# Optimization experiments

Measured on AMD Instinct MI355X. Metric: run time of the kernel, lower is better.

Reference implementation:

```python
import jax, jax.numpy as jnp
import numpy as np

T, B, I, H, L = 1024, 64, 512, 512, 2


def _gru_layer(x_seq, h0, w_ih, w_hh, b_ih, b_hh):
    # x_seq: [T, B, in], h0: [B, H]
    # Precompute input-side gates for all timesteps in one big GEMM.
    gx = jnp.einsum('tbi,gi->tbg', x_seq, w_ih) + b_ih  # [T, B, 3H]

    def step(h, gx_t):
        gh = h @ w_hh.T + b_hh                 # [B, 3H]
        i_r, i_z, i_n = jnp.split(gx_t, 3, axis=-1)
        h_r, h_z, h_n = jnp.split(gh, 3, axis=-1)
        r = jax.nn.sigmoid(i_r + h_r)
        z = jax.nn.sigmoid(i_z + h_z)
        n = jnp.tanh(i_n + r * h_n)
        hy = n + z * (h - n)                   # newgate + inputgate*(hx - newgate)
        return hy, hy

    hT, out = jax.lax.scan(step, h0, gx)
    return out, hT  # out: [T, B, H]


def setup_inputs() -> dict:
    key = jax.random.key(0)
    ks = jax.random.split(key, 10)
    stdv = 1.0 / np.sqrt(H)
    u = lambda k, shp: jax.random.uniform(k, shp, jnp.float32, -stdv, stdv)
    return {
        'x': jax.random.normal(ks[0], (T, B, I), jnp.float32),
        'hx': jax.random.normal(ks[1], (L, B, H), jnp.float32),
        'w_ih_0': u(ks[2], (3 * H, I)),
        'w_hh_0': u(ks[3], (3 * H, H)),
        'b_ih_0': u(ks[4], (3 * H,)),
        'b_hh_0': u(ks[5], (3 * H,)),
        'w_ih_1': u(ks[6], (3 * H, H)),
        'w_hh_1': u(ks[7], (3 * H, H)),
        'b_ih_1': u(ks[8], (3 * H,)),
        'b_hh_1': u(ks[9], (3 * H,)),
    }


def reference(x, hx, w_ih_0, w_hh_0, b_ih_0, b_hh_0, w_ih_1, w_hh_1, b_ih_1, b_hh_1):
    out0, h0T = _gru_layer(x, hx[0], w_ih_0, w_hh_0, b_ih_0, b_hh_0)
    out1, h1T = _gru_layer(out0, hx[1], w_ih_1, w_hh_1, b_ih_1, b_hh_1)
    output = out1                         # [T, B, H] (batch_first=False)
    output_hs = jnp.stack([h0T, h1T], 0)  # [L, B, H]
    return output, output_hs
```

## Files before the change

kernel.cpp:

```cpp
#include <hip/hip_runtime.h>
#include <cstdint>
#include <cstddef>

#define T_N 1024
#define B_N 64
#define I_N 512
#define H_N 512
#define G3  (3*H_N)
#define NBLK 256

typedef _Float16 f16;
typedef _Float16 f16x2 __attribute__((ext_vector_type(2)));

__device__ __forceinline__ f16x2 mkh2(float a, float b) {
  f16x2 v; v.x = (_Float16)a; v.y = (_Float16)b; return v;
}
__device__ __forceinline__ f16x2 bch2(unsigned int u) {
  return __builtin_bit_cast(f16x2, u);
}
__device__ __forceinline__ float fdot2_(f16x2 a, f16x2 b, float c) {
#if __has_builtin(__builtin_amdgcn_fdot2)
  return __builtin_amdgcn_fdot2(a, b, c, false);
#else
  return fmaf((float)a.x, (float)b.x, fmaf((float)a.y, (float)b.y, c));
#endif
}
__device__ __forceinline__ float sigm_(float x) { return 1.f / (1.f + __expf(-x)); }

__global__ __launch_bounds__(256) void gemm_nt(
    const float* __restrict__ A,
    const float* __restrict__ W,
    const float* __restrict__ bias,
    float* __restrict__ C,
    int M, int N, int K)
{
  __shared__ float As[32][68];
  __shared__ float Ws[32][68];
  const int tid = threadIdx.x;
  const int n0 = blockIdx.x * 64;
  const int m0 = blockIdx.y * 64;
  const int ty = tid >> 4;
  const int tx = tid & 15;

  float acc[4][4];
#pragma unroll
  for (int i = 0; i < 4; ++i)
#pragma unroll
    for (int j = 0; j < 4; ++j) acc[i][j] = 0.f;

  for (int k0 = 0; k0 < K; k0 += 32) {
#pragma unroll
    for (int i = 0; i < 2; ++i) {
      int idx = tid + i * 256;
      int r   = idx >> 3;
      int c4  = idx & 7;
      float4 va = *(const float4*)(A + (size_t)(m0 + r) * K + k0 + c4 * 4);
      As[c4*4+0][r] = va.x; As[c4*4+1][r] = va.y;
      As[c4*4+2][r] = va.z; As[c4*4+3][r] = va.w;
      float4 vw = *(const float4*)(W + (size_t)(n0 + r) * K + k0 + c4 * 4);
      Ws[c4*4+0][r] = vw.x; Ws[c4*4+1][r] = vw.y;
      Ws[c4*4+2][r] = vw.z; Ws[c4*4+3][r] = vw.w;
    }
    __syncthreads();
#pragma unroll
    for (int k = 0; k < 32; ++k) {
      float4 a = *(const float4*)&As[k][ty * 4];
      float4 w = *(const float4*)&Ws[k][tx * 4];
      acc[0][0] += a.x*w.x; acc[0][1] += a.x*w.y; acc[0][2] += a.x*w.z; acc[0][3] += a.x*w.w;
      acc[1][0] += a.y*w.x; acc[1][1] += a.y*w.y; acc[1][2] += a.y*w.z; acc[1][3] += a.y*w.w;
      acc[2][0] += a.z*w.x; acc[2][1] += a.z*w.y; acc[2][2] += a.z*w.z; acc[2][3] += a.z*w.w;
      acc[3][0] += a.w*w.x; acc[3][1] += a.w*w.y; acc[3][2] += a.w*w.z; acc[3][3] += a.w*w.w;
    }
    __syncthreads();
  }

  float4 bv = *(const float4*)(bias + n0 + tx * 4);
#pragma unroll
  for (int i = 0; i < 4; ++i) {
    int row = m0 + ty * 4 + i;
    float4 o;
    o.x = acc[i][0] + bv.x; o.y = acc[i][1] + bv.y;
    o.z = acc[i][2] + bv.z; o.w = acc[i][3] + bv.w;
    *(float4*)(C + (size_t)row * N + n0 + tx * 4) = o;
  }
}

__global__ __launch_bounds__(256) void pack_h_init(
    const float* __restrict__ hx, f16* h0x1, f16* h1x1)
{
  int i = blockIdx.x * 256 + threadIdx.x;
  h0x1[i] = (f16)hx[i];
  h1x1[i] = (f16)hx[B_N * H_N + i];
}

__global__ __launch_bounds__(256, 1) void gru_fused(
    const float* __restrict__ gx,
    const float* __restrict__ hx,
    const float* wih1, const float* whh0, const float* whh1,
    const float* bih1, const float* bhh0, const float* bhh1,
    float* __restrict__ out,
    float* __restrict__ hT,
    f16* h0x, f16* h1x,
    int* flags0, int* flags1)
{
  __shared__ f16 sh0[8 * 512];
  __shared__ f16 sh1[8 * 512];
  __shared__ float red[512 * 36];
  __shared__ __align__(8) unsigned short pk[128];

  const int tid = threadIdx.x;
  const int bid = blockIdx.x;
  const int g   = bid & 7;
  const int j   = bid >> 3;
  const int up  = tid >> 5;
  const int s   = tid & 31;

  f16x2 wA[3][2][8];
  f16x2 wX[3][2][8];
  f16x2 wH[3][2][8];
#pragma unroll
  for (int q = 0; q < 3; ++q)
#pragma unroll
    for (int e = 0; e < 2; ++e) {
      const size_t row = (size_t)(q * H_N + 16 * j + 2 * up + e);
      const float* pA = whh0 + row * H_N;
      const float* pX = wih1 + row * H_N;
      const float* pH = whh1 + row * H_N;
#pragma unroll
      for (int c = 0; c < 4; ++c) {
        const int k0 = 8 * s + 2 * c;
        const int k1 = 256 + 8 * s + 2 * c;
        wA[q][e][c]     = mkh2(pA[k0], pA[k0 + 1]);
        wA[q][e][4 + c] = mkh2(pA[k1], pA[k1 + 1]);
        wX[q][e][c]     = mkh2(pX[k0], pX[k0 + 1]);
        wX[q][e][4 + c] = mkh2(pX[k1], pX[k1 + 1]);
        wH[q][e][c]     = mkh2(pH[k0], pH[k0 + 1]);
        wH[q][e][4 + c] = mkh2(pH[k1], pH[k1 + 1]);
      }
    }

  const int gu = tid & 15;
  const int gb8 = tid >> 4;
  float bR0=0,bZ0=0,bN0=0, xR1=0,xZ1=0,xN1=0, hR1=0,hZ1=0,hN1=0, hv0=0, hv1=0;
  if (tid < 128) {
    const int unit = 16 * j + gu;
    const int gbi  = 8 * g + gb8;
    bR0 = bhh0[unit]; bZ0 = bhh0[H_N + unit]; bN0 = bhh0[2 * H_N + unit];
    xR1 = bih1[unit]; xZ1 = bih1[H_N + unit]; xN1 = bih1[2 * H_N + unit];
    hR1 = bhh1[unit]; hZ1 = bhh1[H_N + unit]; hN1 = bhh1[2 * H_N + unit];
    hv0 = hx[(size_t)gbi * H_N + unit];
    hv1 = hx[(size_t)(B_N + gbi) * H_N + unit];
  }

  for (int t = 0; t <= T_N; ++t) {
    float ir0 = 0, iz0 = 0, in0 = 0;
    if (t < T_N && tid < 128) {
      const float* p = gx + ((size_t)t * B_N + 8 * g + gb8) * G3 + 16 * j + gu;
      ir0 = p[0]; iz0 = p[H_N]; in0 = p[2 * H_N];
    }

    if (t > 0) {
      if (tid < 64) {
        int* fp = (tid < 32) ? (flags0 + (8 * tid + g) * 16)
                             : (flags1 + (8 * (tid - 32) + g) * 16);
        const int need = (tid < 32) ? t : (t - 1);
        int spin = 0;
        for (;;) {
          int f = __hip_atomic_load(fp, __ATOMIC_RELAXED, __HIP_MEMORY_SCOPE_AGENT);
          if (__all(f >= need)) break;
          __builtin_amdgcn_s_sleep(1);
          if ((++spin & 1023) == 1023)
            __builtin_amdgcn_fence(__ATOMIC_ACQUIRE, "agent");
        }
      }
      __builtin_amdgcn_sched_barrier(0);
      __syncthreads();
    }

    {
      unsigned long long* s0 = (unsigned long long*)(h0x + (size_t)((t - 1) & 1) * (B_N * H_N) + (size_t)(8 * g) * H_N);
      unsigned long long* s1 = (unsigned long long*)(h1x + (size_t)((t - 2) & 1) * (B_N * H_N) + (size_t)(8 * g) * H_N);
      unsigned long long* d0 = (unsigned long long*)sh0;
      unsigned long long* d1 = (unsigned long long*)sh1;
#pragma unroll
      for (int e = 0; e < 4; ++e) {
        d0[e * 256 + tid] = __hip_atomic_load(s0 + e * 256 + tid, __ATOMIC_RELAXED, __HIP_MEMORY_SCOPE_AGENT);
        d1[e * 256 + tid] = __hip_atomic_load(s1 + e * 256 + tid, __ATOMIC_RELAXED, __HIP_MEMORY_SCOPE_AGENT);
      }
    }
    __syncthreads();

    if (t < T_N) {
      float acc[3][2][8];
#pragma unroll
      for (int q = 0; q < 3; ++q)
#pragma unroll
        for (int e = 0; e < 2; ++e)
#pragma unroll
          for (int bb = 0; bb < 8; ++bb) acc[q][e][bb] = 0.f;

#pragma unroll
      for (int bb = 0; bb < 8; ++bb) {
        uint4 u0 = *(const uint4*)&sh0[bb * 512 + 8 * s];
        uint4 u1 = *(const uint4*)&sh0[bb * 512 + 256 + 8 * s];
        f16x2 h[8] = {bch2(u0.x), bch2(u0.y), bch2(u0.z), bch2(u0.w),
                      bch2(u1.x), bch2(u1.y), bch2(u1.z), bch2(u1.w)};
#pragma unroll
        for (int e = 0; e < 2; ++e) {
          float ar = acc[0][e][bb], az = acc[1][e][bb], an = acc[2][e][bb];
#pragma unroll
          for (int c = 0; c < 8; ++c) {
            ar = fdot2_(wA[0][e][c], h[c], ar);
            az = fdot2_(wA[1][e][c], h[c], az);
            an = fdot2_(wA[2][e][c], h[c], an);
          }
          acc[0][e][bb] = ar; acc[1][e][bb] = az; acc[2][e][bb] = an;
        }
      }
#pragma unroll
      for (int q = 0; q < 3; ++q)
#pragma unroll
        for (int e = 0; e < 2; ++e)
#pragma unroll
          for (int bb = 0; bb < 8; ++bb)
            red[((2 * up + e) + 16 * (q * 8 + bb)) * 36 + s] = acc[q][e][bb];
      __syncthreads();

      if (tid < 128) {
        float sg[3];
#pragma unroll
        for (int q = 0; q < 3; ++q) {
          const float* rp = &red[(size_t)(gu + 16 * (q * 8 + gb8)) * 36];
          float4 a = *(const float4*)(rp + 0),  b4 = *(const float4*)(rp + 4);
          float4 c4 = *(const float4*)(rp + 8), d4 = *(const float4*)(rp + 12);
          float4 a2 = *(const float4*)(rp + 16), b2 = *(const float4*)(rp + 20);
          float4 c2 = *(const float4*)(rp + 24), d2 = *(const float4*)(rp + 28);
          sg[q] = (((a.x+a.y)+(a.z+a.w)) + ((b4.x+b4.y)+(b4.z+b4.w)))
                + (((c4.x+c4.y)+(c4.z+c4.w)) + ((d4.x+d4.y)+(d4.z+d4.w)))
                + (((a2.x+a2.y)+(a2.z+a2.w)) + ((b2.x+b2.y)+(b2.z+b2.w)))
                + (((c2.x+c2.y)+(c2.z+c2.w)) + ((d2.x+d2.y)+(d2.z+d2.w)));
        }
        float r = sigm_(ir0 + sg[0] + bR0);
        float z = sigm_(iz0 + sg[1] + bZ0);
        float n = tanhf(in0 + r * (sg[2] + bN0));
        float hy = n + z * (hv0 - n);
        hv0 = hy;
        pk[gb8 * 16 + gu] = __builtin_bit_cast(unsigned short, (f16)hy);
        if (t == T_N - 1) hT[(size_t)(8 * g + gb8) * H_N + 16 * j + gu] = hy;
      }
      __syncthreads();
      if (tid < 32) {
        const int bb = tid >> 2, qw = tid & 3;
        unsigned long long v = ((const unsigned long long*)pk)[bb * 4 + qw];
        unsigned long long* dp = (unsigned long long*)(h0x + (size_t)(t & 1) * (B_N * H_N) + (size_t)(8 * g + bb) * H_N + 16 * j) + qw;
        __hip_atomic_store(dp, v, __ATOMIC_RELAXED, __HIP_MEMORY_SCOPE_AGENT);
      }
      asm volatile("s_waitcnt vmcnt(0)" ::: "memory");
      __syncthreads();
      if (tid == 0)
        __hip_atomic_store(flags0 + bid * 16, t + 1, __ATOMIC_RELAXED, __HIP_MEMORY_SCOPE_AGENT);
    }

    if (t > 0) {
      float accB[4][2][8];
#pragma unroll
      for (int q = 0; q < 4; ++q)
#pragma unroll
        for (int e = 0; e < 2; ++e)
#pragma unroll
          for (int bb = 0; bb < 8; ++bb) accB[q][e][bb] = 0.f;

#pragma unroll
      for (int bb = 0; bb < 8; ++bb) {
        uint4 ux0 = *(const uint4*)&sh0[bb * 512 + 8 * s];
        uint4 ux1 = *(const uint4*)&sh0[bb * 512 + 256 + 8 * s];
        uint4 uh0 = *(const uint4*)&sh1[bb * 512 + 8 * s];
        uint4 uh1 = *(const uint4*)&sh1[bb * 512 + 256 + 8 * s];
        f16x2 xv[8] = {bch2(ux0.x), bch2(ux0.y), bch2(ux0.z), bch2(ux0.w),
                       bch2(ux1.x), bch2(ux1.y), bch2(ux1.z), bch2(ux1.w)};
        f16x2 hw[8] = {bch2(uh0.x), bch2(uh0.y), bch2(uh0.z), bch2(uh0.w),
                       bch2(uh1.x), bch2(uh1.y), bch2(uh1.z), bch2(uh1.w)};
#pragma unroll
        for (int e = 0; e < 2; ++e) {
          float ar = accB[0][e][bb], az = accB[1][e][bb];
          float anx = accB[2][e][bb], anh = accB[3][e][bb];
#pragma unroll
          for (int c = 0; c < 8; ++c) {
            ar  = fdot2_(wX[0][e][c], xv[c], ar);
            ar  = fdot2_(wH[0][e][c], hw[c], ar);
            az  = fdot2_(wX[1][e][c], xv[c], az);
            az  = fdot2_(wH[1][e][c], hw[c], az);
            anx = fdot2_(wX[2][e][c], xv[c], anx);
            anh = fdot2_(wH[2][e][c], hw[c], anh);
          }
          accB[0][e][bb] = ar;  accB[1][e][bb] = az;
          accB[2][e][bb] = anx; accB[3][e][bb] = anh;
        }
      }
#pragma unroll
      for (int q = 0; q < 4; ++q)
#pragma unroll
        for (int e = 0; e < 2; ++e)
#pragma unroll
          for (int bb = 0; bb < 8; ++bb)
            red[((2 * up + e) + 16 * (q * 8 + bb)) * 36 + s] = accB[q][e][bb];
      __syncthreads();

      float hyB = 0.f;
      if (tid < 128) {
        float sg[4];
#pragma unroll
        for (int q = 0; q < 4; ++q) {
          const float* rp = &red[(size_t)(gu + 16 * (q * 8 + gb8)) * 36];
          float4 a = *(const float4*)(rp + 0),  b4 = *(const float4*)(rp + 4);
          float4 c4 = *(const float4*)(rp + 8), d4 = *(const float4*)(rp + 12);
          float4 a2 = *(const float4*)(rp + 16), b2 = *(const float4*)(rp + 20);
          float4 c2 = *(const float4*)(rp + 24), d2 = *(const float4*)(rp + 28);
          sg[q] = (((a.x+a.y)+(a.z+a.w)) + ((b4.x+b4.y)+(b4.z+b4.w)))
                + (((c4.x+c4.y)+(c4.z+c4.w)) + ((d4.x+d4.y)+(d4.z+d4.w)))
                + (((a2.x+a2.y)+(a2.z+a2.w)) + ((b2.x+b2.y)+(b2.z+b2.w)))
                + (((c2.x+c2.y)+(c2.z+c2.w)) + ((d2.x+d2.y)+(d2.z+d2.w)));
        }
        float r = sigm_(sg[0] + xR1 + hR1);
        float z = sigm_(sg[1] + xZ1 + hZ1);
        float n = tanhf(sg[2] + xN1 + r * (sg[3] + hN1));
        hyB = n + z * (hv1 - n);
        hv1 = hyB;
        pk[gb8 * 16 + gu] = __builtin_bit_cast(unsigned short, (f16)hyB);
      }
      __syncthreads();
      if (tid < 32) {
        const int bb = tid >> 2, qw = tid & 3;
        unsigned long long v = ((const unsigned long long*)pk)[bb * 4 + qw];
        unsigned long long* dp = (unsigned long long*)(h1x + (size_t)((t - 1) & 1) * (B_N * H_N) + (size_t)(8 * g + bb) * H_N + 16 * j) + qw;
        __hip_atomic_store(dp, v, __ATOMIC_RELAXED, __HIP_MEMORY_SCOPE_AGENT);
      }
      asm volatile("s_waitcnt vmcnt(0)" ::: "memory");
      __syncthreads();
      if (tid == 0)
        __hip_atomic_store(flags1 + bid * 16, t, __ATOMIC_RELAXED, __HIP_MEMORY_SCOPE_AGENT);

      if (tid < 128) {
        out[((size_t)(t - 1) * B_N + 8 * g + gb8) * H_N + 16 * j + gu] = hyB;
        if (t == T_N)
          hT[(size_t)(B_N + 8 * g + gb8) * H_N + 16 * j + gu] = hyB;
      }
    }
  }
}

extern "C" void kernel_launch(void* const* d_in, const int* in_sizes, int n_in,
                              void* d_out, int out_size, void* d_ws, size_t ws_size,
                              hipStream_t stream)
{
  const float* x    = (const float*)d_in[0];
  const float* hx   = (const float*)d_in[1];
  const float* wih0 = (const float*)d_in[2];
  const float* whh0 = (const float*)d_in[3];
  const float* bih0 = (const float*)d_in[4];
  const float* bhh0 = (const float*)d_in[5];
  const float* wih1 = (const float*)d_in[6];
  const float* whh1 = (const float*)d_in[7];
  const float* bih1 = (const float*)d_in[8];
  const float* bhh1 = (const float*)d_in[9];
  float* out = (float*)d_out;

  float* gxb = (float*)d_ws;
  f16*   h0x = (f16*)(gxb + (size_t)T_N * B_N * G3);
  f16*   h1x = h0x + 2 * B_N * H_N;
  int*   flags0 = (int*)(h1x + 2 * B_N * H_N);
  int*   flags1 = flags0 + NBLK * 16;

  hipMemsetAsync(flags0, 0, 2 * NBLK * 16 * sizeof(int), stream);
  pack_h_init<<<128, 256, 0, stream>>>(hx, h0x + B_N * H_N, h1x + B_N * H_N);

  dim3 gg(G3 / 64, (T_N * B_N) / 64);
  gemm_nt<<<gg, 256, 0, stream>>>(x, wih0, bih0, gxb, T_N * B_N, G3, I_N);

  gru_fused<<<NBLK, 256, 0, stream>>>(gxb, hx, wih1, whh0, whh1,
                                      bih1, bhh0, bhh1,
                                      out, out + (size_t)T_N * B_N * H_N,
                                      h0x, h1x, flags0, flags1);
}
```

Measured before the change: 10.33 ms.

## Replace flag-based sync with tagged hidden-state data polling and merge layer phases

Drops the per-block flag arrays and instead encodes a parity tag in the low mantissa bit of each f16 hidden-state value, so consumers poll the data itself until the expected tag appears. This removes the separate flag store/load round trip and the waitcnt fences. Both layers' dot products now run in one pass with one shared reduction and one barrier set, with threads 0-127 handling layer 0 and 128-255 handling layer 1 pointwise work. Weights are re-split across 16 lanes per unit instead of 32, and tanh is replaced by a clamped exp formula. The tag bit costs a bit of f16 precision, and correctness relies on relaxed 64-bit atomic stores becoming visible as whole units.

```diff
diff --git a/kernel.cpp b/kernel.cpp
--- a/kernel.cpp
+++ b/kernel.cpp
@@ -11,6 +11,10 @@
 
 typedef _Float16 f16;
 typedef _Float16 f16x2 __attribute__((ext_vector_type(2)));
+typedef unsigned long long ull;
+
+#define SLOT(d) (((d)+2)&1)
+#define TAG1(d) ((((d)+2)>>1)&1)
 
 __device__ __forceinline__ f16x2 mkh2(float a, float b) {
   f16x2 v; v.x = (_Float16)a; v.y = (_Float16)b; return v;
@@ -26,6 +30,11 @@
 #endif
 }
 __device__ __forceinline__ float sigm_(float x) { return 1.f / (1.f + __expf(-x)); }
+__device__ __forceinline__ float tanhf_(float x) {
+  float xx = fminf(15.f, fmaxf(-15.f, x));
+  float e = __expf(2.f * xx);
+  return (e - 1.f) / (e + 1.f);
+}
 
 __global__ __launch_bounds__(256) void gemm_nt(
     const float* __restrict__ A,
@@ -46,7 +55,7 @@
 #pragma unroll
   for (int i = 0; i < 4; ++i)
 #pragma unroll
-    for (int j = 0; j < 4; ++j) acc[i][j] = 0.f;
+    for (int jj = 0; jj < 4; ++jj) acc[i][jj] = 0.f;
 
   for (int k0 = 0; k0 < K; k0 += 32) {
 #pragma unroll
@@ -86,12 +95,20 @@
 }
 
 __global__ __launch_bounds__(256) void pack_h_init(
-    const float* __restrict__ hx, f16* h0x1, f16* h1x1)
+    const float* __restrict__ hx, f16* h0x, f16* h1x)
 {
   int i = blockIdx.x * 256 + threadIdx.x;
-  h0x1[i] = (f16)hx[i];
-  h1x1[i] = (f16)hx[B_N * H_N + i];
-}
+  unsigned short a = __builtin_bit_cast(unsigned short, (f16)hx[i]) & 0xFFFEu;
+  unsigned short b = __builtin_bit_cast(unsigned short, (f16)hx[B_N * H_N + i]) & 0xFFFEu;
+  ((unsigned short*)h0x)[B_N * H_N + i] = a;
+  ((unsigned short*)h1x)[B_N * H_N + i] = b;
+}
+
+#define D4(acc, wv, vv)                      \
+  acc = fdot2_(wv[0], bch2((vv).x), acc);    \
+  acc = fdot2_(wv[1], bch2((vv).y), acc);    \
+  acc = fdot2_(wv[2], bch2((vv).z), acc);    \
+  acc = fdot2_(wv[3], bch2((vv).w), acc);
 
 __global__ __launch_bounds__(256, 1) void gru_fused(
     const float* __restrict__ gx,
@@ -100,250 +117,203 @@
     const float* bih1, const float* bhh0, const float* bhh1,
     float* __restrict__ out,
     float* __restrict__ hT,
-    f16* h0x, f16* h1x,
-    int* flags0, int* flags1)
+    f16* h0x, f16* h1x)
 {
-  __shared__ f16 sh0[8 * 512];
-  __shared__ f16 sh1[8 * 512];
-  __shared__ float red[512 * 36];
-  __shared__ __align__(8) unsigned short pk[128];
+  __shared__ __align__(16) ull sh0q[1024];
+  __shared__ __align__(16) ull sh1q[1024];
+  __shared__ float red[(384 + 512) * 20];
+  __shared__ __align__(8) unsigned short pkA[128], pkB[128];
 
   const int tid = threadIdx.x;
   const int bid = blockIdx.x;
-  const int g   = bid & 7;
-  const int j   = bid >> 3;
-  const int up  = tid >> 5;
-  const int s   = tid & 31;
-
-  f16x2 wA[3][2][8];
-  f16x2 wX[3][2][8];
-  f16x2 wH[3][2][8];
-#pragma unroll
-  for (int q = 0; q < 3; ++q)
-#pragma unroll
-    for (int e = 0; e < 2; ++e) {
-      const size_t row = (size_t)(q * H_N + 16 * j + 2 * up + e);
-      const float* pA = whh0 + row * H_N;
-      const float* pX = wih1 + row * H_N;
-      const float* pH = whh1 + row * H_N;
-#pragma unroll
-      for (int c = 0; c < 4; ++c) {
-        const int k0 = 8 * s + 2 * c;
-        const int k1 = 256 + 8 * s + 2 * c;
-        wA[q][e][c]     = mkh2(pA[k0], pA[k0 + 1]);
-        wA[q][e][4 + c] = mkh2(pA[k1], pA[k1 + 1]);
-        wX[q][e][c]     = mkh2(pX[k0], pX[k0 + 1]);
-        wX[q][e][4 + c] = mkh2(pX[k1], pX[k1 + 1]);
-        wH[q][e][c]     = mkh2(pH[k0], pH[k0 + 1]);
-        wH[q][e][4 + c] = mkh2(pH[k1], pH[k1 + 1]);
-      }
-    }
-
-  const int gu = tid & 15;
-  const int gb8 = tid >> 4;
-  float bR0=0,bZ0=0,bN0=0, xR1=0,xZ1=0,xN1=0, hR1=0,hZ1=0,hN1=0, hv0=0, hv1=0;
-  if (tid < 128) {
-    const int unit = 16 * j + gu;
-    const int gbi  = 8 * g + gb8;
-    bR0 = bhh0[unit]; bZ0 = bhh0[H_N + unit]; bN0 = bhh0[2 * H_N + unit];
-    xR1 = bih1[unit]; xZ1 = bih1[H_N + unit]; xN1 = bih1[2 * H_N + unit];
-    hR1 = bhh1[unit]; hZ1 = bhh1[H_N + unit]; hN1 = bhh1[2 * H_N + unit];
-    hv0 = hx[(size_t)gbi * H_N + unit];
-    hv1 = hx[(size_t)(B_N + gbi) * H_N + unit];
+  const int g = bid & 7;
+  const int j = bid >> 3;
+  const int u = tid >> 4;
+  const int s = tid & 15;
+  const ull M = 0x0001000100010001ULL;
+
+  f16x2 wA[3][4][4], wX[3][4][4], wH[3][4][4];
+#pragma unroll
+  for (int q = 0; q < 3; ++q) {
+    const size_t row = (size_t)(q * H_N + 16 * j + u) * H_N;
+    const float* pA = whh0 + row;
+    const float* pX = wih1 + row;
+    const float* pH = whh1 + row;
+#pragma unroll
+    for (int c = 0; c < 4; ++c)
+#pragma unroll
+      for (int d = 0; d < 4; ++d) {
+        const int k = 8 * s + 128 * c + 2 * d;
+        wA[q][c][d] = mkh2(pA[k], pA[k + 1]);
+        wX[q][c][d] = mkh2(pX[k], pX[k + 1]);
+        wH[q][c][d] = mkh2(pH[k], pH[k + 1]);
+      }
   }
 
+  const int gl = tid & 127, gu = gl & 15, gb8 = gl >> 4;
+  const bool isA = tid < 128;
+  const int unit = 16 * j + gu, gbi = 8 * g + gb8;
+  const float bRv = isA ? bhh0[unit]           : (bih1[unit] + bhh1[unit]);
+  const float bZv = isA ? bhh0[H_N + unit]     : (bih1[H_N + unit] + bhh1[H_N + unit]);
+  const float bNv = isA ? bhh0[2 * H_N + unit] : bih1[2 * H_N + unit];
+  const float bDv = isA ? 0.f                  : bhh1[2 * H_N + unit];
+  float hv = hx[(size_t)(isA ? 0 : B_N * H_N) + (size_t)gbi * H_N + unit];
+
   for (int t = 0; t <= T_N; ++t) {
+    const bool runA = (t < T_N), runB = (t > 0);
+
     float ir0 = 0, iz0 = 0, in0 = 0;
-    if (t < T_N && tid < 128) {
-      const float* p = gx + ((size_t)t * B_N + 8 * g + gb8) * G3 + 16 * j + gu;
+    if (runA && isA) {
+      const float* p = gx + ((size_t)t * B_N + gbi) * G3 + unit;
       ir0 = p[0]; iz0 = p[H_N]; in0 = p[2 * H_N];
     }
 
-    if (t > 0) {
-      if (tid < 64) {
-        int* fp = (tid < 32) ? (flags0 + (8 * tid + g) * 16)
-                             : (flags1 + (8 * (tid - 32) + g) * 16);
-        const int need = (tid < 32) ? t : (t - 1);
-        int spin = 0;
-        for (;;) {
-          int f = __hip_atomic_load(fp, __ATOMIC_RELAXED, __HIP_MEMORY_SCOPE_AGENT);
-          if (__all(f >= need)) break;
-          __builtin_amdgcn_s_sleep(1);
-          if ((++spin & 1023) == 1023)
-            __builtin_amdgcn_fence(__ATOMIC_ACQUIRE, "agent");
+    const ull* s0 = (const ull*)h0x + (size_t)SLOT(t - 1) * 8192 + (size_t)(8 * g) * 128;
+    const ull* s1 = (const ull*)h1x + (size_t)SLOT(t - 2) * 8192 + (size_t)(8 * g) * 128;
+    const ull e0 = TAG1(t - 1) ? M : 0ULL;
+    const ull e1 = TAG1(t - 2) ? M : 0ULL;
+    ull v0[4], v1[4];
+    bool k0[4] = {false, false, false, false};
+    bool k1[4] = {!runB, !runB, !runB, !runB};
+    for (;;) {
+#pragma unroll
+      for (int e = 0; e < 4; ++e) {
+        if (!k0[e]) v0[e] = __hip_atomic_load(s0 + e * 256 + tid, __ATOMIC_RELAXED, __HIP_MEMORY_SCOPE_AGENT);
+        if (!k1[e]) v1[e] = __hip_atomic_load(s1 + e * 256 + tid, __ATOMIC_RELAXED, __HIP_MEMORY_SCOPE_AGENT);
+      }
+      bool all = true;
+#pragma unroll
+      for (int e = 0; e < 4; ++e) {
+        if (!k0[e]) k0[e] = ((v0[e] & M) == e0);
+        if (!k1[e]) k1[e] = ((v1[e] & M) == e1);
+        all = all && k0[e] && k1[e];
+      }
+      if (__all(all)) break;
+      __builtin_amdgcn_s_sleep(1);
+    }
+#pragma unroll
+    for (int e = 0; e < 4; ++e) {
+      sh0q[e * 256 + tid] = v0[e];
+      if (runB) sh1q[e * 256 + tid] = v1[e];
+    }
+    __syncthreads();
+
+    float aA[3][8], aB[4][8];
+#pragma unroll
+    for (int q = 0; q < 3; ++q)
+#pragma unroll
+      for (int bb = 0; bb < 8; ++bb) aA[q][bb] = 0.f;
+#pragma unroll
+    for (int q = 0; q < 4; ++q)
+#pragma unroll
+      for (int bb = 0; bb < 8; ++bb) aB[q][bb] = 0.f;
+
+    const uint4* x4 = (const uint4*)sh0q;
+    const uint4* h4 = (const uint4*)sh1q;
+#pragma unroll
+    for (int bb = 0; bb < 8; ++bb) {
+      uint4 xc[4], hc[4];
+#pragma unroll
+      for (int c = 0; c < 4; ++c) xc[c] = x4[bb * 64 + s + 16 * c];
+      if (runB) {
+#pragma unroll
+        for (int c = 0; c < 4; ++c) hc[c] = h4[bb * 64 + s + 16 * c];
+      }
+      if (runA) {
+#pragma unroll
+        for (int q = 0; q < 3; ++q) {
+          float a = aA[q][bb];
+#pragma unroll
+          for (int c = 0; c < 4; ++c) { D4(a, wA[q][c], xc[c]); }
+          aA[q][bb] = a;
         }
       }
-      __builtin_amdgcn_sched_barrier(0);
-      __syncthreads();
-    }
-
-    {
-      unsigned long long* s0 = (unsigned long long*)(h0x + (size_t)((t - 1) & 1) * (B_N * H_N) + (size_t)(8 * g) * H_N);
-      unsigned long long* s1 = (unsigned long long*)(h1x + (size_t)((t - 2) & 1) * (B_N * H_N) + (size_t)(8 * g) * H_N);
-      unsigned long long* d0 = (unsigned long long*)sh0;
-      unsigned long long* d1 = (unsigned long long*)sh1;
-#pragma unroll
-      for (int e = 0; e < 4; ++e) {
-        d0[e * 256 + tid] = __hip_atomic_load(s0 + e * 256 + tid, __ATOMIC_RELAXED, __HIP_MEMORY_SCOPE_AGENT);
-        d1[e * 256 + tid] = __hip_atomic_load(s1 + e * 256 + tid, __ATOMIC_RELAXED, __HIP_MEMORY_SCOPE_AGENT);
-      }
-    }
-    __syncthreads();
-
-    if (t < T_N) {
-      float acc[3][2][8];
+      if (runB) {
+        float a0 = aB[0][bb], a1 = aB[1][bb], a2 = aB[2][bb], a3 = aB[3][bb];
+#pragma unroll
+        for (int c = 0; c < 4; ++c) {
+          D4(a0, wX[0][c], xc[c]); D4(a0, wH[0][c], hc[c]);
+          D4(a1, wX[1][c], xc[c]); D4(a1, wH[1][c], hc[c]);
+          D4(a2, wX[2][c], xc[c]);
+          D4(a3, wH[2][c], hc[c]);
+        }
+        aB[0][bb] = a0; aB[1][bb] = a1; aB[2][bb] = a2; aB[3][bb] = a3;
+      }
+    }
+
+    const int col = (s + u) & 15;
+    if (runA) {
 #pragma unroll
       for (int q = 0; q < 3; ++q)
 #pragma unroll
-        for (int e = 0; e < 2; ++e)
-#pragma unroll
-          for (int bb = 0; bb < 8; ++bb) acc[q][e][bb] = 0.f;
-
-#pragma unroll
-      for (int bb = 0; bb < 8; ++bb) {
-        uint4 u0 = *(const uint4*)&sh0[bb * 512 + 8 * s];
-        uint4 u1 = *(const uint4*)&sh0[bb * 512 + 256 + 8 * s];
-        f16x2 h[8] = {bch2(u0.x), bch2(u0.y), bch2(u0.z), bch2(u0.w),
-                      bch2(u1.x), bch2(u1.y), bch2(u1.z), bch2(u1.w)};
-#pragma unroll
-        for (int e = 0; e < 2; ++e) {
-          float ar = acc[0][e][bb], az = acc[1][e][bb], an = acc[2][e][bb];
-#pragma unroll
-          for (int c = 0; c < 8; ++c) {
-            ar = fdot2_(wA[0][e][c], h[c], ar);
-            az = fdot2_(wA[1][e][c], h[c], az);
-            an = fdot2_(wA[2][e][c], h[c], an);
-          }
-          acc[0][e][bb] = ar; acc[1][e][bb] = az; acc[2][e][bb] = an;
+        for (int bb = 0; bb < 8; ++bb)
+          red[(size_t)(u + 16 * (q * 8 + bb)) * 20 + col] = aA[q][bb];
+    }
+    if (runB) {
+#pragma unroll
+      for (int q = 0; q < 4; ++q)
+#pragma unroll
+        for (int bb = 0; bb < 8; ++bb)
+          red[(size_t)(384 + u + 16 * (q * 8 + bb)) * 20 + col] = aB[q][bb];
+    }
+    __syncthreads();
+
+    if (isA) {
+      if (runA) {
+        float sg[3];
+#pragma unroll
+        for (int q = 0; q < 3; ++q) {
+          const float* rp = &red[(size_t)(gu + 16 * (q * 8 + gb8)) * 20];
+          float4 a = *(const float4*)rp,        b4 = *(const float4*)(rp + 4);
+          float4 c4 = *(const float4*)(rp + 8), d4 = *(const float4*)(rp + 12);
+          sg[q] = (((a.x + a.y) + (a.z + a.w)) + ((b4.x + b4.y) + (b4.z + b4.w)))
+                + (((c4.x + c4.y) + (c4.z + c4.w)) + ((d4.x + d4.y) + (d4.z + d4.w)));
         }
-      }
-#pragma unroll
-      for (int q = 0; q < 3; ++q)
-#pragma unroll
-        for (int e = 0; e < 2; ++e)
-#pragma unroll
-          for (int bb = 0; bb < 8; ++bb)
-            red[((2 * up + e) + 16 * (q * 8 + bb)) * 36 + s] = acc[q][e][bb];
-      __syncthreads();
-
-      if (tid < 128) {
-        float sg[3];
-#pragma unroll
-        for (int q = 0; q < 3; ++q) {
-          const float* rp = &red[(size_t)(gu + 16 * (q * 8 + gb8)) * 36];
-          float4 a = *(const float4*)(rp + 0),  b4 = *(const float4*)(rp + 4);
+        float r = sigm_(ir0 + sg[0] + bRv);
+        float z = sigm_(iz0 + sg[1] + bZv);
+        float n = tanhf_(in0 + r * (sg[2] + bNv));
+        float hy = n + z * (hv - n); hv = hy;
+        pkA[gl] = __builtin_bit_cast(unsigned short, (f16)hy);
+        if (t == T_N - 1) hT[(size_t)gbi * H_N + unit] = hy;
+      }
+    } else {
+      if (runB) {
+        float sg[4];
+#pragma unroll
+        for (int q = 0; q < 4; ++q) {
+          const float* rp = &red[(size_t)(384 + gu + 16 * (q * 8 + gb8)) * 20];
+          float4 a = *(const float4*)rp,        b4 = *(const float4*)(rp + 4);
           float4 c4 = *(const float4*)(rp + 8), d4 = *(const float4*)(rp + 12);
-          float4 a2 = *(const float4*)(rp + 16), b2 = *(const float4*)(rp + 20);
-          float4 c2 = *(const float4*)(rp + 24), d2 = *(const float4*)(rp + 28);
-          sg[q] = (((a.x+a.y)+(a.z+a.w)) + ((b4.x+b4.y)+(b4.z+b4.w)))
-                + (((c4.x+c4.y)+(c4.z+c4.w)) + ((d4.x+d4.y)+(d4.z+d4.w)))
-                + (((a2.x+a2.y)+(a2.z+a2.w)) + ((b2.x+b2.y)+(b2.z+b2.w)))
-                + (((c2.x+c2.y)+(c2.z+c2.w)) + ((d2.x+d2.y)+(d2.z+d2.w)));
+          sg[q] = (((a.x + a.y) + (a.z + a.w)) + ((b4.x + b4.y) + (b4.z + b4.w)))
+                + (((c4.x + c4.y) + (c4.z + c4.w)) + ((d4.x + d4.y) + (d4.z + d4.w)));
         }
-        float r = sigm_(ir0 + sg[0] + bR0);
-        float z = sigm_(iz0 + sg[1] + bZ0);
-        float n = tanhf(in0 + r * (sg[2] + bN0));
-        float hy = n + z * (hv0 - n);
-        hv0 = hy;
-        pk[gb8 * 16 + gu] = __builtin_bit_cast(unsigned short, (f16)hy);
-        if (t == T_N - 1) hT[(size_t)(8 * g + gb8) * H_N + 16 * j + gu] = hy;
-      }
-      __syncthreads();
-      if (tid < 32) {
-        const int bb = tid >> 2, qw = tid & 3;
-        unsigned long long v = ((const unsigned long long*)pk)[bb * 4 + qw];
-        unsigned long long* dp = (unsigned long long*)(h0x + (size_t)(t & 1) * (B_N * H_N) + (size_t)(8 * g + bb) * H_N + 16 * j) + qw;
+        float r = sigm_(sg[0] + bRv);
+        float z = sigm_(sg[1] + bZv);
+        float n = tanhf_(sg[2] + bNv + r * (sg[3] + bDv));
+        float hy = n + z * (hv - n); hv = hy;
+        pkB[gl] = __builtin_bit_cast(unsigned short, (f16)hy);
+        out[((size_t)(t - 1) * B_N + gbi) * H_N + unit] = hy;
+        if (t == T_N) hT[(size_t)(B_N + gbi) * H_N + unit] = hy;
+      }
+    }
+    __syncthreads();
+
+    if (tid < 32) {
+      if (runA) {
+        ull v = ((const ull*)pkA)[tid];
+        v = (v & ~M) | (TAG1(t) ? M : 0ULL);
+        ull* dp = (ull*)h0x + (size_t)SLOT(t) * 8192
+                + (size_t)(8 * g + (tid >> 2)) * 128 + 4 * j + (tid & 3);
         __hip_atomic_store(dp, v, __ATOMIC_RELAXED, __HIP_MEMORY_SCOPE_AGENT);
       }
-      asm volatile("s_waitcnt vmcnt(0)" ::: "memory");
-      __syncthreads();
-      if (tid == 0)
-        __hip_atomic_store(flags0 + bid * 16, t + 1, __ATOMIC_RELAXED, __HIP_MEMORY_SCOPE_AGENT);
-    }
-
-    if (t > 0) {
-      float accB[4][2][8];
-#pragma unroll
-      for (int q = 0; q < 4; ++q)
-#pragma unroll
-        for (int e = 0; e < 2; ++e)
-#pragma unroll
-          for (int bb = 0; bb < 8; ++bb) accB[q][e][bb] = 0.f;
-
-#pragma unroll
-      for (int bb = 0; bb < 8; ++bb) {
-        uint4 ux0 = *(const uint4*)&sh0[bb * 512 + 8 * s];
-        uint4 ux1 = *(const uint4*)&sh0[bb * 512 + 256 + 8 * s];
-        uint4 uh0 = *(const uint4*)&sh1[bb * 512 + 8 * s];
-        uint4 uh1 = *(const uint4*)&sh1[bb * 512 + 256 + 8 * s];
-        f16x2 xv[8] = {bch2(ux0.x), bch2(ux0.y), bch2(ux0.z), bch2(ux0.w),
-                       bch2(ux1.x), bch2(ux1.y), bch2(ux1.z), bch2(ux1.w)};
-        f16x2 hw[8] = {bch2(uh0.x), bch2(uh0.y), bch2(uh0.z), bch2(uh0.w),
-                       bch2(uh1.x), bch2(uh1.y), bch2(uh1.z), bch2(uh1.w)};
-#pragma unroll
-        for (int e = 0; e < 2; ++e) {
-          float ar = accB[0][e][bb], az = accB[1][e][bb];
-          float anx = accB[2][e][bb], anh = accB[3][e][bb];
-#pragma unroll
-          for (int c = 0; c < 8; ++c) {
-            ar  = fdot2_(wX[0][e][c], xv[c], ar);
-            ar  = fdot2_(wH[0][e][c], hw[c], ar);
-            az  = fdot2_(wX[1][e][c], xv[c], az);
-            az  = fdot2_(wH[1][e][c], hw[c], az);
-            anx = fdot2_(wX[2][e][c], xv[c], anx);
-            anh = fdot2_(wH[2][e][c], hw[c], anh);
-          }
-          accB[0][e][bb] = ar;  accB[1][e][bb] = az;
-          accB[2][e][bb] = anx; accB[3][e][bb] = anh;
-        }
-      }
-#pragma unroll
-      for (int q = 0; q < 4; ++q)
-#pragma unroll
-        for (int e = 0; e < 2; ++e)
-#pragma unroll
-          for (int bb = 0; bb < 8; ++bb)
-            red[((2 * up + e) + 16 * (q * 8 + bb)) * 36 + s] = accB[q][e][bb];
-      __syncthreads();
-
-      float hyB = 0.f;
-      if (tid < 128) {
-        float sg[4];
-#pragma unroll
-        for (int q = 0; q < 4; ++q) {
-          const float* rp = &red[(size_t)(gu + 16 * (q * 8 + gb8)) * 36];
-          float4 a = *(const float4*)(rp + 0),  b4 = *(const float4*)(rp + 4);
-          float4 c4 = *(const float4*)(rp + 8), d4 = *(const float4*)(rp + 12);
-          float4 a2 = *(const float4*)(rp + 16), b2 = *(const float4*)(rp + 20);
-          float4 c2 = *(const float4*)(rp + 24), d2 = *(const float4*)(rp + 28);
-          sg[q] = (((a.x+a.y)+(a.z+a.w)) + ((b4.x+b4.y)+(b4.z+b4.w)))
-                + (((c4.x+c4.y)+(c4.z+c4.w)) + ((d4.x+d4.y)+(d4.z+d4.w)))
-                + (((a2.x+a2.y)+(a2.z+a2.w)) + ((b2.x+b2.y)+(b2.z+b2.w)))
-                + (((c2.x+c2.y)+(c2.z+c2.w)) + ((d2.x+d2.y)+(d2.z+d2.w)));
-        }
-        float r = sigm_(sg[0] + xR1 + hR1);
-        float z = sigm_(sg[1] + xZ1 + hZ1);
-        float n = tanhf(sg[2] + xN1 + r * (sg[3] + hN1));
-        hyB = n + z * (hv1 - n);
-        hv1 = hyB;
-        pk[gb8 * 16 + gu] = __builtin_bit_cast(unsigned short, (f16)hyB);
-      }
-      __syncthreads();
-      if (tid < 32) {
-        const int bb = tid >> 2, qw = tid & 3;
-        unsigned long long v = ((const unsigned long long*)pk)[bb * 4 + qw];
-        unsigned long long* dp = (unsigned long long*)(h1x + (size_t)((t - 1) & 1) * (B_N * H_N) + (size_t)(8 * g + bb) * H_N + 16 * j) + qw;
+    } else if (tid < 64) {
+      if (runB) {
+        const int l = tid - 32;
+        ull v = ((const ull*)pkB)[l];
+        v = (v & ~M) | (TAG1(t - 1) ? M : 0ULL);
+        ull* dp = (ull*)h1x + (size_t)SLOT(t - 1) * 8192
+                + (size_t)(8 * g + (l >> 2)) * 128 + 4 * j + (l & 3);
         __hip_atomic_store(dp, v, __ATOMIC_RELAXED, __HIP_MEMORY_SCOPE_AGENT);
-      }
-      asm volatile("s_waitcnt vmcnt(0)" ::: "memory");
-      __syncthreads();
-      if (tid == 0)
-        __hip_atomic_store(flags1 + bid * 16, t, __ATOMIC_RELAXED, __HIP_MEMORY_SCOPE_AGENT);
-
-      if (tid < 128) {
-        out[((size_t)(t - 1) * B_N + 8 * g + gb8) * H_N + 16 * j + gu] = hyB;
-        if (t == T_N)
-          hT[(size_t)(B_N + 8 * g + gb8) * H_N + 16 * j + gu] = hyB;
       }
     }
   }
@@ -368,11 +338,8 @@
   float* gxb = (float*)d_ws;
   f16*   h0x = (f16*)(gxb + (size_t)T_N * B_N * G3);
   f16*   h1x = h0x + 2 * B_N * H_N;
-  int*   flags0 = (int*)(h1x + 2 * B_N * H_N);
-  int*   flags1 = flags0 + NBLK * 16;
-
-  hipMemsetAsync(flags0, 0, 2 * NBLK * 16 * sizeof(int), stream);
-  pack_h_init<<<128, 256, 0, stream>>>(hx, h0x + B_N * H_N, h1x + B_N * H_N);
+
+  pack_h_init<<<128, 256, 0, stream>>>(hx, h0x, h1x);
 
   dim3 gg(G3 / 64, (T_N * B_N) / 64);
   gemm_nt<<<gg, 256, 0, stream>>>(x, wih0, bih0, gxb, T_N * B_N, G3, I_N);
@@ -380,5 +347,5 @@
   gru_fused<<<NBLK, 256, 0, stream>>>(gxb, hx, wih1, whh0, whh1,
                                       bih1, bhh0, bhh1,
                                       out, out + (size_t)T_N * B_N * H_N,
-                                      h0x, h1x, flags0, flags1);
-}
+                                      h0x, h1x);
+}
```

Result: faster. 8.998 ms (-12.9%).
